# Kernel optimization log

Measured on AMD Instinct MI355X. Metric: run time of the kernel, lower is better.

## Reference

```python
import jax, jax.numpy as jnp
import numpy as np

B, T, D_IN = 4, 512, 4096
H, G, HD = 32, 8, 128            # num_heads, num_kv_groups, head_dim
GS = H // G                      # group_size
CACHE = 3584                     # prev cache length (uniform across batch)
S = CACHE + T                    # total kv length
ROPE_BASE = 10000.0


def _rope_tables(max_pos, head_dim):
    inv_freq = 1.0 / (ROPE_BASE ** (jnp.arange(0, head_dim, 2, dtype=jnp.float32) / head_dim))
    angles = jnp.arange(max_pos, dtype=jnp.float32)[:, None] * inv_freq[None, :]  # [S, hd/2]
    angles = jnp.concatenate([angles, angles], axis=-1)                            # [S, hd]
    return jnp.cos(angles), jnp.sin(angles)


def apply_rope(x, cos, sin, start_positions):
    # x: [B, nH, T, hd]; cos/sin: [S, hd]; start_positions: [B] int
    t = x.shape[2]
    pos = start_positions[:, None] + jnp.arange(t)       # [B, T]
    c = cos[pos][:, None, :, :]                          # [B, 1, T, hd]
    s = sin[pos][:, None, :, :]
    x1, x2 = jnp.split(x, 2, axis=-1)
    rotated = jnp.concatenate([-x2, x1], axis=-1)
    return x * c + rotated * s


def setup_inputs() -> dict:
    key = jax.random.key(0)
    ks = jax.random.split(key, 8)
    x = jax.random.normal(ks[0], (B, T, D_IN), dtype=jnp.float32)
    cos, sin = _rope_tables(S, HD)
    start_positions = jnp.full((B,), CACHE, dtype=jnp.int32)
    # causal mask over absolute positions: query i sits at CACHE+i; True = masked
    kv_pos = jnp.arange(S)[None, None, None, :]
    q_pos = (CACHE + jnp.arange(T))[None, None, :, None]
    mask = jnp.broadcast_to(kv_pos > q_pos, (B, 1, T, S))
    prev_k = jax.random.normal(ks[1], (B, G, CACHE, HD), dtype=jnp.float32)
    prev_v = jax.random.normal(ks[2], (B, G, CACHE, HD), dtype=jnp.float32)
    sc = 0.02
    q_w = jax.random.normal(ks[3], (D_IN, H * HD), dtype=jnp.float32) * sc
    k_w = jax.random.normal(ks[4], (D_IN, G * HD), dtype=jnp.float32) * sc
    v_w = jax.random.normal(ks[5], (D_IN, G * HD), dtype=jnp.float32) * sc
    o_w = jax.random.normal(ks[6], (H * HD, H * HD), dtype=jnp.float32) * sc
    return {"x": x, "mask": mask, "cos": cos, "sin": sin,
            "start_positions": start_positions, "prev_k": prev_k, "prev_v": prev_v,
            "q_w": q_w, "k_w": k_w, "v_w": v_w, "o_w": o_w}


def reference(x, mask, cos, sin, start_positions, prev_k, prev_v, q_w, k_w, v_w, o_w):
    b, t, _ = x.shape
    q = (x @ q_w).reshape(b, t, H, HD).transpose(0, 2, 1, 3)   # [B,H,T,hd]
    k = (x @ k_w).reshape(b, t, G, HD).transpose(0, 2, 1, 3)   # [B,G,T,hd]
    v = (x @ v_w).reshape(b, t, G, HD).transpose(0, 2, 1, 3)   # [B,G,T,hd]
    q = apply_rope(q, cos, sin, start_positions)
    k = apply_rope(k, cos, sin, start_positions)
    # cache concat (uniform lengths -> padded batch concat)
    k_all = jnp.concatenate([prev_k, k], axis=2)               # [B,G,S,hd]
    v_all = jnp.concatenate([prev_v, v], axis=2)
    # GQA expansion: repeat each kv group for its group of query heads
    k_rep = jnp.repeat(k_all, GS, axis=1)                      # [B,H,S,hd]
    v_rep = jnp.repeat(v_all, GS, axis=1)
    scores = jnp.einsum('bhtd,bhsd->bhts', q, k_rep)
    scores = jnp.where(mask, -jnp.inf, scores)
    attn = jax.nn.softmax(scores / jnp.sqrt(jnp.asarray(HD, x.dtype)), axis=-1)
    ctx = jnp.einsum('bhts,bhsd->bthd', attn, v_rep).reshape(b, t, H * HD)
    out = ctx @ o_w
    return out, k_all, v_all
```

## Files before the change

### kernel.cpp

```cpp
#include <hip/hip_runtime.h>

#define B_     4
#define T_     512
#define DIN    4096
#define H_     32
#define G_     8
#define HD_    128
#define S_     4096
#define CACHE_ 3584
#define M_     2048
#define NQKV   6144
#define SCALE  0.08838834764831843f
#define LOG2E  1.4426950408889634f
#define QSC    (SCALE * LOG2E)

typedef __attribute__((ext_vector_type(4)))  float  f32x4;
typedef __attribute__((ext_vector_type(16))) float  f32x16;
typedef __attribute__((ext_vector_type(8)))  short  s16x8;
typedef __attribute__((ext_vector_type(4)))  unsigned short u16x4;
typedef __attribute__((ext_vector_type(8)))  unsigned short u16x8;
typedef __attribute__((ext_vector_type(4)))  unsigned int   u32x4;
typedef unsigned short u16;
typedef unsigned int   u32;

__device__ __forceinline__ u16 f2bf(float f) {
  u32 u = __builtin_bit_cast(u32, f);
  return (u16)((u + 0x7fffu + ((u >> 16) & 1u)) >> 16);
}
__device__ __forceinline__ float bf2f(u16 h) {
  return __builtin_bit_cast(float, (u32)h << 16);
}
__device__ __forceinline__ f32x4 mfma16(s16x8 a, s16x8 b, f32x4 c) {
  return __builtin_amdgcn_mfma_f32_16x16x32_bf16(a, b, c, 0, 0, 0);
}
__device__ __forceinline__ u32 pkbf(float a, float b) {
  u32 r; asm("v_cvt_pk_bf16_f32 %0, %1, %2" : "=v"(r) : "v"(a), "v"(b)); return r;
}
__device__ __forceinline__ void gload_lds16(const void* g, void* l) {
  __builtin_amdgcn_global_load_lds((__attribute__((address_space(1))) void*)g,
                                   (__attribute__((address_space(3))) void*)l, 16, 0, 0);
}

__global__ __launch_bounds__(256) void k_prep_w(const float* __restrict__ qw, const float* __restrict__ kw,
                                                const float* __restrict__ vw, const float* __restrict__ ow,
                                                const float* __restrict__ x,
                                                u16* __restrict__ wt_qkv, u16* __restrict__ wt_o,
                                                u16* __restrict__ xb) {
  const int bx = blockIdx.x, by = blockIdx.y, t = threadIdx.x;
  if (by >= 160) {
    size_t i = (((size_t)(by - 160) * 64 + bx) * 256 + t) * 4;
    f32x4 v = *(const f32x4*)(x + i);
    u16x4 o = { f2bf(v[0]), f2bf(v[1]), f2bf(v[2]), f2bf(v[3]) };
    *(u16x4*)(xb + i) = o;
    return;
  }
  __shared__ float tile[64][68];
  const float* src; u16* dst; int ldn, n0;
  if (by < 64)      { src = qw; ldn = 4096; dst = wt_qkv;                         n0 = by * 64; }
  else if (by < 80) { src = kw; ldn = 1024; dst = wt_qkv + (size_t)4096 * 4096;   n0 = (by - 64) * 64; }
  else if (by < 96) { src = vw; ldn = 1024; dst = wt_qkv + (size_t)5120 * 4096;   n0 = (by - 80) * 64; }
  else              { src = ow; ldn = 4096; dst = wt_o;                           n0 = (by - 96) * 64; }
  const int k0 = bx * 64;
  int rr = t >> 4, cc = (t & 15) * 4;
#pragma unroll
  for (int p = 0; p < 4; ++p) {
    int r = p * 16 + rr;
    f32x4 v = *(const f32x4*)(src + (size_t)(k0 + r) * ldn + n0 + cc);
    tile[r][cc] = v[0]; tile[r][cc + 1] = v[1]; tile[r][cc + 2] = v[2]; tile[r][cc + 3] = v[3];
  }
  __syncthreads();
#pragma unroll
  for (int p = 0; p < 4; ++p) {
    int n = p * 16 + rr;
    u16x4 o = { f2bf(tile[cc][n]), f2bf(tile[cc + 1][n]), f2bf(tile[cc + 2][n]), f2bf(tile[cc + 3][n]) };
    *(u16x4*)(dst + (size_t)(n0 + n) * 4096 + k0 + cc) = o;
  }
}

__global__ __launch_bounds__(256) void k_prep_kv(const float* __restrict__ pk, const float* __restrict__ pv,
                                                 float* __restrict__ k_all, float* __restrict__ v_all,
                                                 u16* __restrict__ kb, u16* __restrict__ vt) {
  __shared__ float tile[64][132];
  const int bg = blockIdx.y, t = threadIdx.x;
  if (blockIdx.x < 448) {
    size_t si = ((size_t)blockIdx.x * 256 + t) * 4;
    f32x4 v = *(const f32x4*)(pk + (size_t)bg * CACHE_ * HD_ + si);
    size_t dof = (size_t)bg * S_ * HD_ + si;
    *(f32x4*)(k_all + dof) = v;
    u16x4 o = { f2bf(v[0]), f2bf(v[1]), f2bf(v[2]), f2bf(v[3]) };
    *(u16x4*)(kb + dof) = o;
    return;
  }
  const int s0 = (blockIdx.x - 448) * 64;
  const float* src = pv + ((size_t)bg * CACHE_ + s0) * HD_;
  float* dc = v_all + ((size_t)bg * S_ + s0) * HD_;
  int r8 = t >> 5, c4 = (t & 31) * 4;
#pragma unroll
  for (int p = 0; p < 8; ++p) {
    int r = p * 8 + r8;
    f32x4 v = *(const f32x4*)(src + (size_t)r * HD_ + c4);
    *(f32x4*)(dc + (size_t)r * HD_ + c4) = v;
    tile[r][c4] = v[0]; tile[r][c4 + 1] = v[1]; tile[r][c4 + 2] = v[2]; tile[r][c4 + 3] = v[3];
  }
  __syncthreads();
  int hr = t >> 4, s4 = (t & 15) * 4;
#pragma unroll
  for (int p = 0; p < 8; ++p) {
    int hd = p * 16 + hr;
    u16x4 o = { f2bf(tile[s4][hd]), f2bf(tile[s4 + 1][hd]), f2bf(tile[s4 + 2][hd]), f2bf(tile[s4 + 3][hd]) };
    *(u16x4*)(vt + ((size_t)bg * HD_ + hd) * S_ + s0 + s4) = o;
  }
}

template<int BM, int BN, bool OUT_F32>
__global__ __launch_bounds__(512, 1) void k_gemm2(const u16* __restrict__ A, const u16* __restrict__ Bt,
                                                  void* __restrict__ Cp, int M, int N, int K) {
  constexpr int MI = BM / 32;
  constexpr int NI = BN / 64;
  constexpr int LA = BM / 64;
  constexpr int VM = LA + NI;
  __shared__ u16 As[2 * BM * 64];
  __shared__ u16 Bs[2 * BN * 64];
  const int tid = threadIdx.x, w = tid >> 6, lane = tid & 63;
  const int wr = w >> 2, wc = w & 3;
  const int cl = lane & 15, khi = lane >> 4;
  const int Mt = M / BM;
  const int nwg = gridDim.x;
  const int q = nwg >> 3, r8 = nwg & 7;
  const int xcd = blockIdx.x & 7, pos = blockIdx.x >> 3;
  const int wgid = (xcd < r8 ? xcd * (q + 1) : r8 * (q + 1) + (xcd - r8) * q) + pos;
  const int m0 = (wgid % Mt) * BM, n0 = (wgid / Mt) * BN;
  const int rb = tid >> 3;
  const int csw = ((tid & 7) ^ (rb & 7)) * 8;
  const u16* aS = A  + (size_t)(m0 + rb) * K + csw;
  const u16* bS = Bt + (size_t)(n0 + rb) * K + csw;
  u16* aD = As + w * 512;
  u16* bD = Bs + w * 512;
  const int ck0 = ((0 + khi) ^ (cl & 7)) * 8;
  const int ck1 = ((4 + khi) ^ (cl & 7)) * 8;
  const int NT = K >> 6;
  f32x4 acc[MI][NI] = {};

#define STAGE_(buf, tt)                                                                   \
  do {                                                                                    \
    _Pragma("unroll")                                                                     \
    for (int i = 0; i < LA; ++i)                                                          \
      gload_lds16(aS + (size_t)(i * 64) * K + (size_t)(tt) * 64, aD + (buf) * (BM * 64) + i * 4096); \
    _Pragma("unroll")                                                                     \
    for (int i = 0; i < NI; ++i)                                                          \
      gload_lds16(bS + (size_t)(i * 64) * K + (size_t)(tt) * 64, bD + (buf) * (BN * 64) + i * 4096); \
  } while (0)
#define VMCNT_L_()                                                                        \
  do {                                                                                    \
    if constexpr (VM == 8)      asm volatile("s_waitcnt vmcnt(8)" ::: "memory");          \
    else if constexpr (VM == 7) asm volatile("s_waitcnt vmcnt(7)" ::: "memory");          \
    else                        asm volatile("s_waitcnt vmcnt(6)" ::: "memory");          \
  } while (0)

  STAGE_(0, 0);
  STAGE_(1, 1);
  VMCNT_L_();
  __builtin_amdgcn_sched_barrier(0);
  __builtin_amdgcn_s_barrier();
  __builtin_amdgcn_sched_barrier(0);

  for (int t = 0; t < NT; ++t) {
    const int buf = t & 1;
    const int ab = buf * (BM * 64) + (wr * (BM / 2) + cl) * 64;
    const int bb = buf * (BN * 64) + (wc * (BN / 4) + cl) * 64;
#pragma unroll
    for (int kk = 0; kk < 2; ++kk) {
      const int ck = kk ? ck1 : ck0;
      s16x8 bf4[NI], af[MI];
#pragma unroll
      for (int ni = 0; ni < NI; ++ni) bf4[ni] = *(const s16x8*)(Bs + bb + ni * 16 * 64 + ck);
#pragma unroll
      for (int mi = 0; mi < MI; ++mi) af[mi] = *(const s16x8*)(As + ab + mi * 16 * 64 + ck);
      __builtin_amdgcn_s_setprio(1);
#pragma unroll
      for (int mi = 0; mi < MI; ++mi)
#pragma unroll
        for (int ni = 0; ni < NI; ++ni)
          acc[mi][ni] = mfma16(af[mi], bf4[ni], acc[mi][ni]);
      __builtin_amdgcn_s_setprio(0);
    }
    __builtin_amdgcn_sched_barrier(0);
    __builtin_amdgcn_s_barrier();
    __builtin_amdgcn_sched_barrier(0);
    if (t + 2 < NT) STAGE_(buf, t + 2);
    VMCNT_L_();
    __builtin_amdgcn_sched_barrier(0);
    __builtin_amdgcn_s_barrier();
    __builtin_amdgcn_sched_barrier(0);
  }
#undef STAGE_
#undef VMCNT_L_
  const int rl = khi * 4;
#pragma unroll
  for (int mi = 0; mi < MI; ++mi)
#pragma unroll
    for (int ni = 0; ni < NI; ++ni) {
      int col = n0 + wc * (BN / 4) + ni * 16 + cl;
#pragma unroll
      for (int r = 0; r < 4; ++r) {
        int rw = m0 + wr * (BM / 2) + mi * 16 + rl + r;
        if (OUT_F32) ((float*)Cp)[(size_t)rw * N + col] = acc[mi][ni][r];
        else         ((u16*)Cp)[(size_t)rw * N + col]   = f2bf(acc[mi][ni][r]);
      }
    }
}

__global__ __launch_bounds__(256) void k_rope(const u16* __restrict__ qkv, const float* __restrict__ cosT,
                                              const float* __restrict__ sinT, const int* __restrict__ sp,
                                              u16* __restrict__ qr, u16* __restrict__ kb,
                                              float* __restrict__ k_all, float* __restrict__ v_all) {
  int bt = blockIdx.x;
  int b = bt >> 9, t = bt & 511;
  int pos = sp[b] + t;
  const u16* row = qkv + (size_t)bt * NQKV;
  for (int idx = threadIdx.x; idx < 2560; idx += 256) {
    int head = idx >> 6, d = idx & 63;
    float c = cosT[pos * HD_ + d], s = sinT[pos * HD_ + d];
    float x1 = bf2f(row[head * HD_ + d]);
    float x2 = bf2f(row[head * HD_ + d + 64]);
    float y1 = x1 * c - x2 * s;
    float y2 = x2 * c + x1 * s;
    if (head < 32) {
      size_t o = (((size_t)b * H_ + head) * T_ + t) * HD_ + d;
      qr[o] = f2bf(y1 * QSC); qr[o + 64] = f2bf(y2 * QSC);
    } else {
      int g = head - 32;
      size_t o = (((size_t)b * G_ + g) * S_ + CACHE_ + t) * HD_ + d;
      kb[o] = f2bf(y1); kb[o + 64] = f2bf(y2);
      k_all[o] = y1; k_all[o + 64] = y2;
    }
  }
  for (int idx = threadIdx.x; idx < 1024; idx += 256) {
    int g = idx >> 7;
    float v = bf2f(row[5120 + idx]);
    size_t o = (((size_t)b * G_ + g) * S_ + CACHE_ + t) * HD_ + (idx & 127);
    v_all[o] = v;
  }
}

__global__ __launch_bounds__(256) void k_tv_new(const u16* __restrict__ qkv, u16* __restrict__ vt) {
  __shared__ u16 tile[64][72];
  int bg = blockIdx.y;
  int b = bg >> 3, g = bg & 7;
  int tt = blockIdx.x >> 1, ht = blockIdx.x & 1;
  int t0 = tt * 64, hd0 = ht * 64;
  int t = threadIdx.x;
  int rr = t >> 3, c8 = (t & 7) * 8;
#pragma unroll
  for (int p = 0; p < 2; ++p) {
    int r = p * 32 + rr;
    *(u16x8*)(&tile[r][c8]) =
      *(const u16x8*)(qkv + (size_t)(b * T_ + t0 + r) * NQKV + 5120 + g * HD_ + hd0 + c8);
  }
  __syncthreads();
  int hr = t >> 4, s4 = (t & 15) * 4;
#pragma unroll
  for (int p = 0; p < 4; ++p) {
    int hd = p * 16 + hr;
    u16x4 o = { tile[s4][hd], tile[s4 + 1][hd], tile[s4 + 2][hd], tile[s4 + 3][hd] };
    *(u16x4*)(vt + ((size_t)bg * HD_ + hd0 + hd) * S_ + CACHE_ + t0 + s4) = o;
  }
}

__global__ __launch_bounds__(512) void k_attn(const u16* __restrict__ Q, const u16* __restrict__ Kc,
                                              const u16* __restrict__ Vt, const int* __restrict__ sp,
                                              u16* __restrict__ ctx) {
  __shared__ u16 Ks[2][64 * 128];
  __shared__ u16 Vs[2][128 * 64];
  const int xcd = blockIdx.x & 7, pos = blockIdx.x >> 3;
  const int wgid = xcd * 32 + pos;
  const int qh = wgid & 1, hq = (wgid >> 1) & 3, bg = wgid >> 3;
  const int b = bg >> 3, g = bg & 7, h = g * 4 + hq;
  const int tid = threadIdx.x, w = tid >> 6, lane = tid & 63;
  const int l31 = lane & 31, hh = lane >> 5;
  const int cache = sp[b];
  const int qbase = qh * 256;
  const int qtok = qbase + w * 32 + l31;
  const size_t kvoff = (size_t)bg * S_ * HD_;
  const u16* kp = Kc + kvoff;
  const u16* vp = Vt + kvoff;
  s16x8 qreg[8];
  {
    const u16* qb = Q + ((size_t)(b * H_ + h) * T_ + qtok) * HD_;
#pragma unroll
    for (int s = 0; s < 8; ++s) qreg[s] = *(const s16x8*)(qb + s * 16 + hh * 8);
  }
  f32x16 acc[4] = {};
  float mr = -1e30f, ls = 0.f;
  const int krow = w * 8 + (lane >> 3), kch = lane & 7;
  const int vrow = w * 16 + (lane >> 2), vch = lane & 3;
  const int kswz = (krow & 15) << 3;
  const int vswz = (vrow & 7) << 3;
  const int rdswzK = (l31 & 15) << 3;
  const int rdswzV = (l31 & 7) << 3;
  const int jm = (cache + qbase + w * 32) >> 6;
  const int jlastB = (cache + qbase + 255) >> 6;
  const int kvlim = cache + qtok;
  u16x8 rk0, rk1, rv0, rv1;
  rk0 = *(const u16x8*)(kp + (size_t)krow * HD_ + kch * 8);
  rk1 = *(const u16x8*)(kp + (size_t)krow * HD_ + (kch + 8) * 8);
  rv0 = *(const u16x8*)(vp + (size_t)vrow * S_ + vch * 8);
  rv1 = *(const u16x8*)(vp + (size_t)vrow * S_ + (vch + 4) * 8);
  *(u16x8*)(Ks[0] + krow * 128 + ((kch * 8) ^ kswz))       = rk0;
  *(u16x8*)(Ks[0] + krow * 128 + (((kch + 8) * 8) ^ kswz)) = rk1;
  *(u16x8*)(Vs[0] + vrow * 64 + ((vch * 8) ^ vswz))        = rv0;
  *(u16x8*)(Vs[0] + vrow * 64 + (((vch + 4) * 8) ^ vswz))  = rv1;
  rk0 = *(const u16x8*)(kp + (size_t)(64 + krow) * HD_ + kch * 8);
  rk1 = *(const u16x8*)(kp + (size_t)(64 + krow) * HD_ + (kch + 8) * 8);
  rv0 = *(const u16x8*)(vp + (size_t)vrow * S_ + 64 + vch * 8);
  rv1 = *(const u16x8*)(vp + (size_t)vrow * S_ + 64 + (vch + 4) * 8);
  __syncthreads();
  for (int j = 0; j <= jlastB; ++j) {
    const int buf = j & 1;
    const u16* KsB = Ks[buf];
    const u16* VsB = Vs[buf];
    u16* Ksn = Ks[buf ^ 1];
    u16* Vsn = Vs[buf ^ 1];
    f32x16 sa[2] = {};
    __builtin_amdgcn_s_setprio(1);
#pragma unroll
    for (int s = 0; s < 8; ++s) {
      s16x8 ka = *(const s16x8*)(KsB + l31 * 128 + ((s * 16 + hh * 8) ^ rdswzK));
      sa[0] = __builtin_amdgcn_mfma_f32_32x32x16_bf16(ka, qreg[s], sa[0], 0, 0, 0);
    }
#pragma unroll
    for (int s = 0; s < 8; ++s) {
      s16x8 ka = *(const s16x8*)(KsB + (32 + l31) * 128 + ((s * 16 + hh * 8) ^ rdswzK));
      sa[1] = __builtin_amdgcn_mfma_f32_32x32x16_bf16(ka, qreg[s], sa[1], 0, 0, 0);
    }
    __builtin_amdgcn_s_setprio(0);
    if (j < jlastB) {
      *(u16x8*)(Ksn + krow * 128 + ((kch * 8) ^ kswz))       = rk0;
      *(u16x8*)(Ksn + krow * 128 + (((kch + 8) * 8) ^ kswz)) = rk1;
      *(u16x8*)(Vsn + vrow * 64 + ((vch * 8) ^ vswz))        = rv0;
      *(u16x8*)(Vsn + vrow * 64 + (((vch + 4) * 8) ^ vswz))  = rv1;
    }
    if (j + 2 <= jlastB) {
      rk0 = *(const u16x8*)(kp + (size_t)((j + 2) * 64 + krow) * HD_ + kch * 8);
      rk1 = *(const u16x8*)(kp + (size_t)((j + 2) * 64 + krow) * HD_ + (kch + 8) * 8);
      rv0 = *(const u16x8*)(vp + (size_t)vrow * S_ + (j + 2) * 64 + vch * 8);
      rv1 = *(const u16x8*)(vp + (size_t)vrow * S_ + (j + 2) * 64 + (vch + 4) * 8);
    }
    if (j >= jm) {
#pragma unroll
      for (int r = 0; r < 16; ++r) {
        int kv = j * 64 + (r & 3) + 8 * (r >> 2) + 4 * hh;
        if (kv > kvlim)      sa[0][r] = -1e30f;
        if (kv + 32 > kvlim) sa[1][r] = -1e30f;
      }
    }
    float mx;
    {
      float t[16];
#pragma unroll
      for (int r = 0; r < 16; ++r) t[r] = fmaxf(sa[0][r], sa[1][r]);
#define F3_(a, b, c) fmaxf(fmaxf(a, b), c)
      float u0 = F3_(t[0], t[1], t[2]);
      float u1 = F3_(t[3], t[4], t[5]);
      float u2 = F3_(t[6], t[7], t[8]);
      float u3 = F3_(t[9], t[10], t[11]);
      float u4 = F3_(t[12], t[13], t[14]);
      float lm = fmaxf(F3_(u0, u1, u2), F3_(u3, u4, t[15]));
#undef F3_
      mx = fmaxf(lm, __shfl_xor(lm, 32));
    }
    if (__any(mx > mr + 8.f)) {
      float nm = fmaxf(mr, mx);
      float al = __builtin_amdgcn_exp2f(mr - nm);
      mr = nm; ls *= al;
#pragma unroll
      for (int r = 0; r < 16; ++r) {
        float ar = __shfl(al, (r & 3) + 8 * (r >> 2) + 4 * hh, 64);
        acc[0][r] *= ar; acc[1][r] *= ar; acc[2][r] *= ar; acc[3][r] *= ar;
      }
    }
    float p0 = 0.f, p1 = 0.f, p2 = 0.f, p3 = 0.f, p4 = 0.f, p5 = 0.f, p6 = 0.f, p7 = 0.f;
#pragma unroll
    for (int r = 0; r < 16; r += 4) {
      float e0 = __builtin_amdgcn_exp2f(sa[0][r]     - mr);
      float e1 = __builtin_amdgcn_exp2f(sa[0][r + 1] - mr);
      float e2 = __builtin_amdgcn_exp2f(sa[0][r + 2] - mr);
      float e3 = __builtin_amdgcn_exp2f(sa[0][r + 3] - mr);
      sa[0][r] = e0; sa[0][r + 1] = e1; sa[0][r + 2] = e2; sa[0][r + 3] = e3;
      p0 += e0; p1 += e1; p2 += e2; p3 += e3;
    }
#pragma unroll
    for (int r = 0; r < 16; r += 4) {
      float e0 = __builtin_amdgcn_exp2f(sa[1][r]     - mr);
      float e1 = __builtin_amdgcn_exp2f(sa[1][r + 1] - mr);
      float e2 = __builtin_amdgcn_exp2f(sa[1][r + 2] - mr);
      float e3 = __builtin_amdgcn_exp2f(sa[1][r + 3] - mr);
      sa[1][r] = e0; sa[1][r + 1] = e1; sa[1][r + 2] = e2; sa[1][r + 3] = e3;
      p4 += e0; p5 += e1; p6 += e2; p7 += e3;
    }
    float rsum = ((p0 + p1) + (p2 + p3)) + ((p4 + p5) + (p6 + p7));
    ls += rsum + __shfl_xor(rsum, 32);
    s16x8 pf[4];
#pragma unroll
    for (int sb = 0; sb < 2; ++sb) {
      u32 a0 = pkbf(sa[sb][0],  sa[sb][1]),  a1 = pkbf(sa[sb][2],  sa[sb][3]);
      u32 b0 = pkbf(sa[sb][4],  sa[sb][5]),  b1 = pkbf(sa[sb][6],  sa[sb][7]);
      u32 c0 = pkbf(sa[sb][8],  sa[sb][9]),  c1 = pkbf(sa[sb][10], sa[sb][11]);
      u32 d0 = pkbf(sa[sb][12], sa[sb][13]), d1 = pkbf(sa[sb][14], sa[sb][15]);
      u32 xa0 = __shfl_xor(a0, 32), xa1 = __shfl_xor(a1, 32);
      u32 xb0 = __shfl_xor(b0, 32), xb1 = __shfl_xor(b1, 32);
      u32 xc0 = __shfl_xor(c0, 32), xc1 = __shfl_xor(c1, 32);
      u32 xd0 = __shfl_xor(d0, 32), xd1 = __shfl_xor(d1, 32);
      u32x4 f0 = { hh ? xb0 : a0, hh ? xb1 : a1, hh ? b0 : xa0, hh ? b1 : xa1 };
      u32x4 f1 = { hh ? xd0 : c0, hh ? xd1 : c1, hh ? d0 : xc0, hh ? d1 : xc1 };
      pf[sb * 2]     = __builtin_bit_cast(s16x8, f0);
      pf[sb * 2 + 1] = __builtin_bit_cast(s16x8, f1);
    }
    __builtin_amdgcn_s_setprio(1);
#pragma unroll
    for (int hb = 0; hb < 4; ++hb) {
      const int vro = hb * 32 + l31;
#pragma unroll
      for (int kb = 0; kb < 4; ++kb) {
        s16x8 vb = *(const s16x8*)(VsB + vro * 64 + ((kb * 16 + hh * 8) ^ rdswzV));
        acc[hb] = __builtin_amdgcn_mfma_f32_32x32x16_bf16(pf[kb], vb, acc[hb], 0, 0, 0);
      }
    }
    __builtin_amdgcn_s_setprio(0);
    __syncthreads();
  }
  float inv = 1.0f / ls;
#pragma unroll
  for (int r = 0; r < 16; ++r) {
    int ql = (r & 3) + 8 * (r >> 2) + 4 * hh;
    float ivr = __shfl(inv, ql, 64);
    u16* cb = ctx + ((size_t)(b * T_ + qbase + w * 32 + ql)) * 4096 + h * HD_ + l31;
    cb[0]  = f2bf(acc[0][r] * ivr);
    cb[32] = f2bf(acc[1][r] * ivr);
    cb[64] = f2bf(acc[2][r] * ivr);
    cb[96] = f2bf(acc[3][r] * ivr);
  }
}

extern "C" void kernel_launch(void* const* d_in, const int* in_sizes, int n_in,
                              void* d_out, int out_size, void* d_ws, size_t ws_size,
                              hipStream_t stream) {
  const float* x      = (const float*)d_in[0];
  const float* cosT   = (const float*)d_in[2];
  const float* sinT   = (const float*)d_in[3];
  const int*   sp     = (const int*)d_in[4];
  const float* prev_k = (const float*)d_in[5];
  const float* prev_v = (const float*)d_in[6];
  const float* q_w    = (const float*)d_in[7];
  const float* k_w    = (const float*)d_in[8];
  const float* v_w    = (const float*)d_in[9];
  const float* o_w    = (const float*)d_in[10];

  float* out   = (float*)d_out;
  float* k_all = out + (size_t)B_ * T_ * H_ * HD_;
  float* v_all = k_all + (size_t)B_ * G_ * S_ * HD_;

  char* w = (char*)d_ws;
  u16* wt_qkv = (u16*)(w);
  u16* wt_o   = (u16*)(w + 50331648);
  u16* x_bf   = (u16*)(w + 83886080);
  u16* qkv_bf = (u16*)(w + 100663296);
  u16* q_rope = (u16*)(w + 125829120);
  u16* k_bf   = (u16*)(w + 142606336);
  u16* v_t    = (u16*)(w + 176160768);
  u16* ctx    = (u16*)(w + 209715200);
  if (ws_size < 226492416ull) return;

  k_prep_w<<<dim3(64, 288), 256, 0, stream>>>(q_w, k_w, v_w, o_w, x, wt_qkv, wt_o, x_bf);
  k_prep_kv<<<dim3(504, 32), 256, 0, stream>>>(prev_k, prev_v, k_all, v_all, k_bf, v_t);
  k_gemm2<256, 192, false><<<256, 512, 0, stream>>>(x_bf, wt_qkv, qkv_bf, M_, NQKV, 4096);
  k_rope<<<2048, 256, 0, stream>>>(qkv_bf, cosT, sinT, sp, q_rope, k_bf, k_all, v_all);
  k_tv_new<<<dim3(16, 32), 256, 0, stream>>>(qkv_bf, v_t);
  k_attn<<<256, 512, 0, stream>>>(q_rope, k_bf, v_t, sp, ctx);
  k_gemm2<128, 256, true><<<256, 512, 0, stream>>>(ctx, wt_o, out, M_, 4096, 4096);
}
```

Baseline: 508.2 us.

## Split attention softmax into two 32-key halves and vectorize RoPE kernel

The flash-attention inner loop now does masking, max, rescale, exp, pack and PV MFMAs separately for each 32-key sub-block, instead of one pass over the 64-key tile. This is meant to let the PV MFMAs for the first half overlap with the softmax math of the second half, at the cost of an extra max/rescale check and shuffle reduction per tile. The RoPE kernel is also rewritten to use 4-wide vector loads and stores for cos/sin, q/k and v, which cuts the number of memory instructions.

```diff
diff --git a/kernel.cpp b/kernel.cpp
--- a/kernel.cpp
+++ b/kernel.cpp
@@ -218,28 +218,44 @@
   int b = bt >> 9, t = bt & 511;
   int pos = sp[b] + t;
   const u16* row = qkv + (size_t)bt * NQKV;
-  for (int idx = threadIdx.x; idx < 2560; idx += 256) {
-    int head = idx >> 6, d = idx & 63;
-    float c = cosT[pos * HD_ + d], s = sinT[pos * HD_ + d];
-    float x1 = bf2f(row[head * HD_ + d]);
-    float x2 = bf2f(row[head * HD_ + d + 64]);
-    float y1 = x1 * c - x2 * s;
-    float y2 = x2 * c + x1 * s;
+  const float* cp = cosT + (size_t)pos * HD_;
+  const float* sq = sinT + (size_t)pos * HD_;
+  for (int hp = threadIdx.x; hp < 640; hp += 256) {
+    int head = hp >> 4, q4 = (hp & 15) * 4;
+    f32x4 c = *(const f32x4*)(cp + q4);
+    f32x4 s = *(const f32x4*)(sq + q4);
+    u16x4 xa = *(const u16x4*)(row + head * HD_ + q4);
+    u16x4 xb = *(const u16x4*)(row + head * HD_ + q4 + 64);
+    f32x4 y1, y2;
+#pragma unroll
+    for (int e = 0; e < 4; ++e) {
+      float x1 = bf2f(xa[e]), x2 = bf2f(xb[e]);
+      y1[e] = x1 * c[e] - x2 * s[e];
+      y2[e] = x2 * c[e] + x1 * s[e];
+    }
     if (head < 32) {
-      size_t o = (((size_t)b * H_ + head) * T_ + t) * HD_ + d;
-      qr[o] = f2bf(y1 * QSC); qr[o + 64] = f2bf(y2 * QSC);
+      size_t o = (((size_t)b * H_ + head) * T_ + t) * HD_ + q4;
+      u16x4 o1 = { f2bf(y1[0] * QSC), f2bf(y1[1] * QSC), f2bf(y1[2] * QSC), f2bf(y1[3] * QSC) };
+      u16x4 o2 = { f2bf(y2[0] * QSC), f2bf(y2[1] * QSC), f2bf(y2[2] * QSC), f2bf(y2[3] * QSC) };
+      *(u16x4*)(qr + o) = o1;
+      *(u16x4*)(qr + o + 64) = o2;
     } else {
       int g = head - 32;
-      size_t o = (((size_t)b * G_ + g) * S_ + CACHE_ + t) * HD_ + d;
-      kb[o] = f2bf(y1); kb[o + 64] = f2bf(y2);
-      k_all[o] = y1; k_all[o + 64] = y2;
-    }
-  }
-  for (int idx = threadIdx.x; idx < 1024; idx += 256) {
-    int g = idx >> 7;
-    float v = bf2f(row[5120 + idx]);
-    size_t o = (((size_t)b * G_ + g) * S_ + CACHE_ + t) * HD_ + (idx & 127);
-    v_all[o] = v;
+      size_t o = (((size_t)b * G_ + g) * S_ + CACHE_ + t) * HD_ + q4;
+      u16x4 o1 = { f2bf(y1[0]), f2bf(y1[1]), f2bf(y1[2]), f2bf(y1[3]) };
+      u16x4 o2 = { f2bf(y2[0]), f2bf(y2[1]), f2bf(y2[2]), f2bf(y2[3]) };
+      *(u16x4*)(kb + o) = o1;
+      *(u16x4*)(kb + o + 64) = o2;
+      *(f32x4*)(k_all + o) = y1;
+      *(f32x4*)(k_all + o + 64) = y2;
+    }
+  }
+  {
+    int vq = threadIdx.x;
+    int g = vq >> 5, d4 = (vq & 31) * 4;
+    u16x4 v = *(const u16x4*)(row + 5120 + g * HD_ + d4);
+    f32x4 vf = { bf2f(v[0]), bf2f(v[1]), bf2f(v[2]), bf2f(v[3]) };
+    *(f32x4*)(v_all + (((size_t)b * G_ + g) * S_ + CACHE_ + t) * HD_ + d4) = vf;
   }
 }
 
@@ -346,87 +362,76 @@
       rv0 = *(const u16x8*)(vp + (size_t)vrow * S_ + (j + 2) * 64 + vch * 8);
       rv1 = *(const u16x8*)(vp + (size_t)vrow * S_ + (j + 2) * 64 + (vch + 4) * 8);
     }
-    if (j >= jm) {
-#pragma unroll
-      for (int r = 0; r < 16; ++r) {
-        int kv = j * 64 + (r & 3) + 8 * (r >> 2) + 4 * hh;
-        if (kv > kvlim)      sa[0][r] = -1e30f;
-        if (kv + 32 > kvlim) sa[1][r] = -1e30f;
-      }
-    }
-    float mx;
-    {
-      float t[16];
-#pragma unroll
-      for (int r = 0; r < 16; ++r) t[r] = fmaxf(sa[0][r], sa[1][r]);
+#pragma unroll
+    for (int sb = 0; sb < 2; ++sb) {
+      if (j >= jm) {
+#pragma unroll
+        for (int r = 0; r < 16; ++r) {
+          int kv = j * 64 + sb * 32 + (r & 3) + 8 * (r >> 2) + 4 * hh;
+          if (kv > kvlim) sa[sb][r] = -1e30f;
+        }
+      }
+      float mx;
+      {
+        float* t = (float*)&sa[sb];
 #define F3_(a, b, c) fmaxf(fmaxf(a, b), c)
-      float u0 = F3_(t[0], t[1], t[2]);
-      float u1 = F3_(t[3], t[4], t[5]);
-      float u2 = F3_(t[6], t[7], t[8]);
-      float u3 = F3_(t[9], t[10], t[11]);
-      float u4 = F3_(t[12], t[13], t[14]);
-      float lm = fmaxf(F3_(u0, u1, u2), F3_(u3, u4, t[15]));
+        float u0 = F3_(t[0], t[1], t[2]);
+        float u1 = F3_(t[3], t[4], t[5]);
+        float u2 = F3_(t[6], t[7], t[8]);
+        float u3 = F3_(t[9], t[10], t[11]);
+        float u4 = F3_(t[12], t[13], t[14]);
+        float lm = fmaxf(F3_(u0, u1, u2), F3_(u3, u4, t[15]));
 #undef F3_
-      mx = fmaxf(lm, __shfl_xor(lm, 32));
-    }
-    if (__any(mx > mr + 8.f)) {
-      float nm = fmaxf(mr, mx);
-      float al = __builtin_amdgcn_exp2f(mr - nm);
-      mr = nm; ls *= al;
-#pragma unroll
-      for (int r = 0; r < 16; ++r) {
-        float ar = __shfl(al, (r & 3) + 8 * (r >> 2) + 4 * hh, 64);
-        acc[0][r] *= ar; acc[1][r] *= ar; acc[2][r] *= ar; acc[3][r] *= ar;
-      }
-    }
-    float p0 = 0.f, p1 = 0.f, p2 = 0.f, p3 = 0.f, p4 = 0.f, p5 = 0.f, p6 = 0.f, p7 = 0.f;
-#pragma unroll
-    for (int r = 0; r < 16; r += 4) {
-      float e0 = __builtin_amdgcn_exp2f(sa[0][r]     - mr);
-      float e1 = __builtin_amdgcn_exp2f(sa[0][r + 1] - mr);
-      float e2 = __builtin_amdgcn_exp2f(sa[0][r + 2] - mr);
-      float e3 = __builtin_amdgcn_exp2f(sa[0][r + 3] - mr);
-      sa[0][r] = e0; sa[0][r + 1] = e1; sa[0][r + 2] = e2; sa[0][r + 3] = e3;
-      p0 += e0; p1 += e1; p2 += e2; p3 += e3;
-    }
-#pragma unroll
-    for (int r = 0; r < 16; r += 4) {
-      float e0 = __builtin_amdgcn_exp2f(sa[1][r]     - mr);
-      float e1 = __builtin_amdgcn_exp2f(sa[1][r + 1] - mr);
-      float e2 = __builtin_amdgcn_exp2f(sa[1][r + 2] - mr);
-      float e3 = __builtin_amdgcn_exp2f(sa[1][r + 3] - mr);
-      sa[1][r] = e0; sa[1][r + 1] = e1; sa[1][r + 2] = e2; sa[1][r + 3] = e3;
-      p4 += e0; p5 += e1; p6 += e2; p7 += e3;
-    }
-    float rsum = ((p0 + p1) + (p2 + p3)) + ((p4 + p5) + (p6 + p7));
-    ls += rsum + __shfl_xor(rsum, 32);
-    s16x8 pf[4];
-#pragma unroll
-    for (int sb = 0; sb < 2; ++sb) {
-      u32 a0 = pkbf(sa[sb][0],  sa[sb][1]),  a1 = pkbf(sa[sb][2],  sa[sb][3]);
-      u32 b0 = pkbf(sa[sb][4],  sa[sb][5]),  b1 = pkbf(sa[sb][6],  sa[sb][7]);
-      u32 c0 = pkbf(sa[sb][8],  sa[sb][9]),  c1 = pkbf(sa[sb][10], sa[sb][11]);
-      u32 d0 = pkbf(sa[sb][12], sa[sb][13]), d1 = pkbf(sa[sb][14], sa[sb][15]);
-      u32 xa0 = __shfl_xor(a0, 32), xa1 = __shfl_xor(a1, 32);
-      u32 xb0 = __shfl_xor(b0, 32), xb1 = __shfl_xor(b1, 32);
-      u32 xc0 = __shfl_xor(c0, 32), xc1 = __shfl_xor(c1, 32);
-      u32 xd0 = __shfl_xor(d0, 32), xd1 = __shfl_xor(d1, 32);
-      u32x4 f0 = { hh ? xb0 : a0, hh ? xb1 : a1, hh ? b0 : xa0, hh ? b1 : xa1 };
-      u32x4 f1 = { hh ? xd0 : c0, hh ? xd1 : c1, hh ? d0 : xc0, hh ? d1 : xc1 };
-      pf[sb * 2]     = __builtin_bit_cast(s16x8, f0);
-      pf[sb * 2 + 1] = __builtin_bit_cast(s16x8, f1);
-    }
-    __builtin_amdgcn_s_setprio(1);
-#pragma unroll
-    for (int hb = 0; hb < 4; ++hb) {
-      const int vro = hb * 32 + l31;
-#pragma unroll
-      for (int kb = 0; kb < 4; ++kb) {
-        s16x8 vb = *(const s16x8*)(VsB + vro * 64 + ((kb * 16 + hh * 8) ^ rdswzV));
-        acc[hb] = __builtin_amdgcn_mfma_f32_32x32x16_bf16(pf[kb], vb, acc[hb], 0, 0, 0);
-      }
-    }
-    __builtin_amdgcn_s_setprio(0);
+        mx = fmaxf(lm, __shfl_xor(lm, 32));
+      }
+      if (__any(mx > mr + 8.f)) {
+        float nm = fmaxf(mr, mx);
+        float al = __builtin_amdgcn_exp2f(mr - nm);
+        mr = nm; ls *= al;
+#pragma unroll
+        for (int r = 0; r < 16; ++r) {
+          float ar = __shfl(al, (r & 3) + 8 * (r >> 2) + 4 * hh, 64);
+          acc[0][r] *= ar; acc[1][r] *= ar; acc[2][r] *= ar; acc[3][r] *= ar;
+        }
+      }
+      float p0 = 0.f, p1 = 0.f, p2 = 0.f, p3 = 0.f;
+#pragma unroll
+      for (int r = 0; r < 16; r += 4) {
+        float e0 = __builtin_amdgcn_exp2f(sa[sb][r]     - mr);
+        float e1 = __builtin_amdgcn_exp2f(sa[sb][r + 1] - mr);
+        float e2 = __builtin_amdgcn_exp2f(sa[sb][r + 2] - mr);
+        float e3 = __builtin_amdgcn_exp2f(sa[sb][r + 3] - mr);
+        sa[sb][r] = e0; sa[sb][r + 1] = e1; sa[sb][r + 2] = e2; sa[sb][r + 3] = e3;
+        p0 += e0; p1 += e1; p2 += e2; p3 += e3;
+      }
+      float rsum = (p0 + p1) + (p2 + p3);
+      ls += rsum + __shfl_xor(rsum, 32);
+      s16x8 pf0, pf1;
+      {
+        u32 a0 = pkbf(sa[sb][0],  sa[sb][1]),  a1 = pkbf(sa[sb][2],  sa[sb][3]);
+        u32 b0 = pkbf(sa[sb][4],  sa[sb][5]),  b1 = pkbf(sa[sb][6],  sa[sb][7]);
+        u32 c0 = pkbf(sa[sb][8],  sa[sb][9]),  c1 = pkbf(sa[sb][10], sa[sb][11]);
+        u32 d0 = pkbf(sa[sb][12], sa[sb][13]), d1 = pkbf(sa[sb][14], sa[sb][15]);
+        u32 xa0 = __shfl_xor(a0, 32), xa1 = __shfl_xor(a1, 32);
+        u32 xb0 = __shfl_xor(b0, 32), xb1 = __shfl_xor(b1, 32);
+        u32 xc0 = __shfl_xor(c0, 32), xc1 = __shfl_xor(c1, 32);
+        u32 xd0 = __shfl_xor(d0, 32), xd1 = __shfl_xor(d1, 32);
+        u32x4 f0 = { hh ? xb0 : a0, hh ? xb1 : a1, hh ? b0 : xa0, hh ? b1 : xa1 };
+        u32x4 f1 = { hh ? xd0 : c0, hh ? xd1 : c1, hh ? d0 : xc0, hh ? d1 : xc1 };
+        pf0 = __builtin_bit_cast(s16x8, f0);
+        pf1 = __builtin_bit_cast(s16x8, f1);
+      }
+      __builtin_amdgcn_s_setprio(1);
+#pragma unroll
+      for (int hb = 0; hb < 4; ++hb) {
+        const int vro = hb * 32 + l31;
+        s16x8 vb0 = *(const s16x8*)(VsB + vro * 64 + (((sb * 2) * 16 + hh * 8) ^ rdswzV));
+        s16x8 vb1 = *(const s16x8*)(VsB + vro * 64 + (((sb * 2 + 1) * 16 + hh * 8) ^ rdswzV));
+        acc[hb] = __builtin_amdgcn_mfma_f32_32x32x16_bf16(pf0, vb0, acc[hb], 0, 0, 0);
+        acc[hb] = __builtin_amdgcn_mfma_f32_32x32x16_bf16(pf1, vb1, acc[hb], 0, 0, 0);
+      }
+      __builtin_amdgcn_s_setprio(0);
+    }
     __syncthreads();
   }
   float inv = 1.0f / ls;
```

Result: no change. 507.1 us (median of 2 runs) (-0.2%).
